# Kernel optimization log

Hardware: AMD Instinct MI355X
Metric: run time of the kernel (lower is better)

The kernel has to match this reference:

```python
import jax, jax.numpy as jnp
import numpy as np


def setup_inputs() -> dict:
    key = jax.random.key(0)
    k1, k2, k3, k4 = jax.random.split(key, 4)
    B, T, N, C_IN, C_OUT, K = 32, 24, 1024, 64, 64, 3
    x = jax.random.normal(k1, (B, T, N, C_IN), dtype=jnp.float32)
    Tks = jax.random.normal(k2, (K, N, N), dtype=jnp.float32)
    # kaiming-uniform-ish init scale for Theta, small uniform bias
    bound_t = float(np.sqrt(6.0 / C_IN))
    Theta = jax.random.uniform(k3, (K, C_IN, C_OUT), dtype=jnp.float32,
                               minval=-bound_t, maxval=bound_t)
    bound_b = 1.0 / float(np.sqrt(C_IN))
    bias = jax.random.uniform(k4, (K, C_OUT), dtype=jnp.float32,
                              minval=-bound_b, maxval=bound_b)
    return {"x": x, "Tks": Tks, "Theta": Theta, "bias": bias}


def reference(x, Tks, Theta, bias):
    # torch.einsum('nn,btnc->btnc', T_k, x) extracts diag(T_k) and scales x per node.
    d = jnp.diagonal(Tks, axis1=1, axis2=2)  # [K, N]
    # sum_k diag(T_k) * x @ Theta_k  -> [B, T, N, C_OUT]
    out = jnp.einsum('kn,btnc,kco->btno', d, x, Theta)
    # each bias[k] is added once -> total additive term is sum over k
    out = out + jnp.sum(bias, axis=0)
    return out
```

## Files before the change

kernel.cpp:

```cpp
#include <hip/hip_runtime.h>


#define NNODES 1024
#define ROWS_PER_BLOCK 256
#define NBLOCKS 3072
#define ITERS 4

typedef __attribute__((ext_vector_type(8))) short  short8;
typedef __attribute__((ext_vector_type(4))) float  f32x4;

__device__ __forceinline__ unsigned short f2bf(float f) {
    union { float f; unsigned u; } v; v.f = f;
    unsigned r = v.u + 0x7FFFu + ((v.u >> 16) & 1u);
    return (unsigned short)(r >> 16);
}

__global__ __launch_bounds__(256, 4) void cheb_flat(
    const float* __restrict__ x,
    const float* __restrict__ Tks,
    const float* __restrict__ Theta,
    const float* __restrict__ bias,
    float* __restrict__ out)
{
    __shared__ __align__(16) unsigned short WT[3][64][72];
    __shared__ __align__(16) float d4[ROWS_PER_BLOCK][4];
    __shared__ float bsum[64];

    const int tid = threadIdx.x;
    const int rowbase = blockIdx.x * ROWS_PER_BLOCK;

    for (int idx = tid; idx < 3 * 64 * 16; idx += 256) {
        const int k   = idx >> 10;
        const int rem = idx & 1023;
        const int c   = rem >> 4;
        const int og  = (rem & 15) << 2;
        const f32x4 th = *reinterpret_cast<const f32x4*>(Theta + k * 4096 + c * 64 + og);
        WT[k][og + 0][c] = f2bf(th[0]);
        WT[k][og + 1][c] = f2bf(th[1]);
        WT[k][og + 2][c] = f2bf(th[2]);
        WT[k][og + 3][c] = f2bf(th[3]);
    }
    for (int r = tid; r < ROWS_PER_BLOCK; r += 256) {
        const int n = (rowbase + r) & (NNODES - 1);
        const size_t diag = (size_t)n * (NNODES + 1);
        f32x4 v;
        v[0] = Tks[diag];
        v[1] = Tks[(size_t)NNODES * NNODES + diag];
        v[2] = Tks[(size_t)2 * NNODES * NNODES + diag];
        v[3] = 0.0f;
        *reinterpret_cast<f32x4*>(&d4[r][0]) = v;
    }
    if (tid < 64) bsum[tid] = bias[tid] + bias[64 + tid] + bias[128 + tid];
    __syncthreads();

    const int wave = tid >> 6;
    const int lane = tid & 63;
    const int lrow = lane & 15;
    const int lgrp = lane >> 4;

    float bs[4];
    #pragma unroll
    for (int nb = 0; nb < 4; ++nb) bs[nb] = bsum[nb * 16 + lrow];

    #pragma unroll 1
    for (int it = 0; it < ITERS; ++it) {
        const int lr  = it * 64 + wave * 16 + lrow;
        const float* xrow = x + (size_t)(rowbase + lr) * 64;

        const f32x4 x0 = *reinterpret_cast<const f32x4*>(xrow + lgrp * 8);
        const f32x4 x1 = *reinterpret_cast<const f32x4*>(xrow + lgrp * 8 + 4);
        const f32x4 x2 = *reinterpret_cast<const f32x4*>(xrow + 32 + lgrp * 8);
        const f32x4 x3 = *reinterpret_cast<const f32x4*>(xrow + 32 + lgrp * 8 + 4);

        const f32x4 dv = *reinterpret_cast<const f32x4*>(&d4[lr][0]);

        short8 af[6];
        #pragma unroll
        for (int k = 0; k < 3; ++k) {
            const float dk = dv[k];
            #pragma unroll
            for (int j = 0; j < 4; ++j) {
                af[k * 2    ][j]     = (short)f2bf(dk * x0[j]);
                af[k * 2    ][4 + j] = (short)f2bf(dk * x1[j]);
                af[k * 2 + 1][j]     = (short)f2bf(dk * x2[j]);
                af[k * 2 + 1][4 + j] = (short)f2bf(dk * x3[j]);
            }
        }

        f32x4 acc[4] = {f32x4{0,0,0,0}, f32x4{0,0,0,0}, f32x4{0,0,0,0}, f32x4{0,0,0,0}};
        #pragma unroll
        for (int k = 0; k < 3; ++k) {
            #pragma unroll
            for (int h = 0; h < 2; ++h) {
                #pragma unroll
                for (int nb = 0; nb < 4; ++nb) {
                    const unsigned short* bp = &WT[k][nb * 16 + lrow][h * 32 + lgrp * 8];
                    const short8 bf = *reinterpret_cast<const short8*>(bp);
                    acc[nb] = __builtin_amdgcn_mfma_f32_16x16x32_bf16(af[k * 2 + h], bf, acc[nb], 0, 0, 0);
                }
            }
        }

        const int orow = rowbase + it * 64 + wave * 16 + lgrp * 4;
        #pragma unroll
        for (int nb = 0; nb < 4; ++nb) {
            const float bv = bs[nb];
            const size_t obase = (size_t)orow * 64 + nb * 16 + lrow;
            #pragma unroll
            for (int j = 0; j < 4; ++j) {
                out[obase + (size_t)j * 64] = acc[nb][j] + bv;
            }
        }
        __syncthreads();
    }
}

extern "C" void kernel_launch(void* const* d_in, const int* in_sizes, int n_in,
                              void* d_out, int out_size, void* d_ws, size_t ws_size,
                              hipStream_t stream) {
    const float* x     = (const float*)d_in[0];
    const float* Tks   = (const float*)d_in[1];
    const float* Theta = (const float*)d_in[2];
    const float* bias  = (const float*)d_in[3];
    float* out = (float*)d_out;

    hipLaunchKernelGGL(cheb_flat, dim3(NBLOCKS), dim3(256), 0, stream,
                       x, Tks, Theta, bias, out);
}
```

Baseline: 92.35 us.

## Hoist weight fragments to registers, swap MFMA operands for vectorized stores

The Theta bf16 fragments are loaded from shared memory into registers once per block instead of on every iteration. The MFMA operands are swapped so each lane's accumulator holds four consecutive output columns of one row, which allows 16-byte vector stores instead of strided scalar stores. The per-iteration __syncthreads and the occupancy hint in launch_bounds are dropped. The trade-off is higher register pressure, since 24 short8 weight fragments stay resident, which may reduce occupancy.

```diff
diff --git a/kernel.cpp b/kernel.cpp
--- a/kernel.cpp
+++ b/kernel.cpp
@@ -15,7 +15,7 @@
     return (unsigned short)(r >> 16);
 }
 
-__global__ __launch_bounds__(256, 4) void cheb_flat(
+__global__ __launch_bounds__(256) void cheb_v3(
     const float* __restrict__ x,
     const float* __restrict__ Tks,
     const float* __restrict__ Theta,
@@ -24,7 +24,7 @@
 {
     __shared__ __align__(16) unsigned short WT[3][64][72];
     __shared__ __align__(16) float d4[ROWS_PER_BLOCK][4];
-    __shared__ float bsum[64];
+    __shared__ __align__(16) float bsum[64];
 
     const int tid = threadIdx.x;
     const int rowbase = blockIdx.x * ROWS_PER_BLOCK;
@@ -40,7 +40,8 @@
         WT[k][og + 2][c] = f2bf(th[2]);
         WT[k][og + 3][c] = f2bf(th[3]);
     }
-    for (int r = tid; r < ROWS_PER_BLOCK; r += 256) {
+    {
+        const int r = tid;
         const int n = (rowbase + r) & (NNODES - 1);
         const size_t diag = (size_t)n * (NNODES + 1);
         f32x4 v;
@@ -58,13 +59,24 @@
     const int lrow = lane & 15;
     const int lgrp = lane >> 4;
 
-    float bs[4];
+    short8 wf[3][2][4];
     #pragma unroll
-    for (int nb = 0; nb < 4; ++nb) bs[nb] = bsum[nb * 16 + lrow];
+    for (int kc = 0; kc < 3; ++kc)
+        #pragma unroll
+        for (int h = 0; h < 2; ++h)
+            #pragma unroll
+            for (int nb = 0; nb < 4; ++nb)
+                wf[kc][h][nb] = *reinterpret_cast<const short8*>(
+                    &WT[kc][nb * 16 + lrow][h * 32 + lgrp * 8]);
+
+    f32x4 bs4[4];
+    #pragma unroll
+    for (int nb = 0; nb < 4; ++nb)
+        bs4[nb] = *reinterpret_cast<const f32x4*>(&bsum[nb * 16 + lgrp * 4]);
 
     #pragma unroll 1
     for (int it = 0; it < ITERS; ++it) {
-        const int lr  = it * 64 + wave * 16 + lrow;
+        const int lr = it * 64 + wave * 16 + lrow;
         const float* xrow = x + (size_t)(rowbase + lr) * 64;
 
         const f32x4 x0 = *reinterpret_cast<const f32x4*>(xrow + lgrp * 8);
@@ -74,44 +86,37 @@
 
         const f32x4 dv = *reinterpret_cast<const f32x4*>(&d4[lr][0]);
 
-        short8 af[6];
+        short8 xf[3][2];
         #pragma unroll
-        for (int k = 0; k < 3; ++k) {
-            const float dk = dv[k];
+        for (int kc = 0; kc < 3; ++kc) {
+            const float dk = dv[kc];
             #pragma unroll
             for (int j = 0; j < 4; ++j) {
-                af[k * 2    ][j]     = (short)f2bf(dk * x0[j]);
-                af[k * 2    ][4 + j] = (short)f2bf(dk * x1[j]);
-                af[k * 2 + 1][j]     = (short)f2bf(dk * x2[j]);
-                af[k * 2 + 1][4 + j] = (short)f2bf(dk * x3[j]);
+                xf[kc][0][j]     = (short)f2bf(dk * x0[j]);
+                xf[kc][0][4 + j] = (short)f2bf(dk * x1[j]);
+                xf[kc][1][j]     = (short)f2bf(dk * x2[j]);
+                xf[kc][1][4 + j] = (short)f2bf(dk * x3[j]);
             }
         }
 
         f32x4 acc[4] = {f32x4{0,0,0,0}, f32x4{0,0,0,0}, f32x4{0,0,0,0}, f32x4{0,0,0,0}};
         #pragma unroll
-        for (int k = 0; k < 3; ++k) {
+        for (int kc = 0; kc < 3; ++kc)
             #pragma unroll
-            for (int h = 0; h < 2; ++h) {
+            for (int h = 0; h < 2; ++h)
                 #pragma unroll
-                for (int nb = 0; nb < 4; ++nb) {
-                    const unsigned short* bp = &WT[k][nb * 16 + lrow][h * 32 + lgrp * 8];
-                    const short8 bf = *reinterpret_cast<const short8*>(bp);
-                    acc[nb] = __builtin_amdgcn_mfma_f32_16x16x32_bf16(af[k * 2 + h], bf, acc[nb], 0, 0, 0);
-                }
-            }
-        }
+                for (int nb = 0; nb < 4; ++nb)
+                    acc[nb] = __builtin_amdgcn_mfma_f32_16x16x32_bf16(
+                        wf[kc][h][nb], xf[kc][h], acc[nb], 0, 0, 0);
 
-        const int orow = rowbase + it * 64 + wave * 16 + lgrp * 4;
+        float* orow = out + (size_t)(rowbase + lr) * 64;
         #pragma unroll
         for (int nb = 0; nb < 4; ++nb) {
-            const float bv = bs[nb];
-            const size_t obase = (size_t)orow * 64 + nb * 16 + lrow;
+            f32x4 o4;
             #pragma unroll
-            for (int j = 0; j < 4; ++j) {
-                out[obase + (size_t)j * 64] = acc[nb][j] + bv;
-            }
+            for (int j = 0; j < 4; ++j) o4[j] = acc[nb][j] + bs4[nb][j];
+            *reinterpret_cast<f32x4*>(orow + nb * 16 + lgrp * 4) = o4;
         }
-        __syncthreads();
     }
 }
 
@@ -124,6 +129,6 @@
     const float* bias  = (const float*)d_in[3];
     float* out = (float*)d_out;
 
-    hipLaunchKernelGGL(cheb_flat, dim3(NBLOCKS), dim3(256), 0, stream,
+    hipLaunchKernelGGL(cheb_v3, dim3(NBLOCKS), dim3(256), 0, stream,
                        x, Tks, Theta, bias, out);
 }
```

Result: slower. 108.8 us (+17.8%).
